# Kernel tuning notes

Measured on AMD Instinct MI355X. Metric: run time of the kernel, lower is better.

Reference implementation:

```python
import jax, jax.numpy as jnp
import numpy as np

N = 2048          # recurrent units (args_dict['n'])
B = 128           # batch
T = 1024          # timesteps
INHIB_PROP = 0.2  # args_dict['inhib_proportion']
SAT_LO, SAT_HI = 0.0, 1.0e8  # saturations -> effectively ReLU


def setup_inputs() -> dict:
    key = jax.random.key(0)
    ks = jax.random.split(key, 8)
    std = 1.0 / np.sqrt(N)
    x0 = jax.random.normal(ks[0], (B, T), jnp.float32)
    x1 = jax.random.normal(ks[1], (B, T), jnp.float32)
    enc0 = jax.random.normal(ks[2], (N,), jnp.float32) * std
    enc1 = jax.random.normal(ks[3], (N,), jnp.float32) * std
    dec0 = jax.random.normal(ks[4], (N,), jnp.float32) * std
    dec1 = jax.random.normal(ks[5], (N,), jnp.float32) * std
    # Dale constraint: W must be elementwise non-negative (asserted in integrate).
    # Scale 1/N keeps the effective spectral radius < 1 for a stable recurrence.
    W = jax.random.uniform(ks[6], (N, N), jnp.float32) * (1.0 / N)
    n_inhib = int(N * INHIB_PROP)
    signs = jnp.concatenate([jnp.ones(N - n_inhib, jnp.float32),
                             -jnp.ones(n_inhib, jnp.float32)])
    mask = jnp.ones((N,), jnp.float32)
    state0 = jnp.zeros((N,), jnp.float32)
    return {"x0": x0, "x1": x1, "enc0": enc0, "enc1": enc1,
            "dec0": dec0, "dec1": dec1, "W": W, "signs": signs,
            "mask": mask, "state0": state0}


def reference(x0, x1, enc0, enc1, dec0, dec1, W, signs, mask, state0):
    # Effective recurrent matrix: W @ diag(signs); state update uses its transpose.
    Weff_T = (W * signs[None, :]).T  # [N, N]

    def step(state, xt):  # state: [B, N]
        i0, i1 = xt  # each [B]
        ext = enc0[None, :] * i0[:, None] + enc1[None, :] * i1[:, None]  # [B, N]
        new_state = mask * jnp.clip((state + mask * ext) @ Weff_T, SAT_LO, SAT_HI)
        o0 = (dec0 * new_state).sum(-1)  # [B]
        o1 = (dec1 * new_state).sum(-1)  # [B]
        return new_state, (o0, o1)

    init = jnp.broadcast_to(state0, (x0.shape[0], state0.shape[0]))  # [B, N]
    _, (o0, o1) = jax.lax.scan(step, init, (x0.T, x1.T))  # outputs [T, B]
    return o0.T, o1.T  # each [B, T]
```

## Files before the change

### kernel.cpp

```cpp
#include <hip/hip_runtime.h>
#include <hip/hip_bf16.h>
#include <stdint.h>


#define NN 2048
#define BB 128
#define TT 1024

typedef __attribute__((ext_vector_type(8)))  __bf16          bf16x8;
typedef __attribute__((ext_vector_type(8)))  unsigned short  ushort8;
typedef __attribute__((ext_vector_type(16))) float           f32x16;

#define IF_OFF   0u
#define IF_FRAGS 32768
#define CTR_OFF  (1u << 20)
#define CTR_BYTES (1024u * 4u * 16u * 4u)

__device__ __forceinline__ unsigned short f2bf(float f) {
    __hip_bfloat16 h = __float2bfloat16(f);
    return *reinterpret_cast<unsigned short*>(&h);
}

__global__ void init_pack(const float* __restrict__ x0, const float* __restrict__ x1,
                          const float* __restrict__ enc0, const float* __restrict__ enc1,
                          const float* __restrict__ mask, const float* __restrict__ state0,
                          unsigned short* __restrict__ If)
{
    int idx  = blockIdx.x * 256 + threadIdx.x;
    int e    = idx & 7;
    int lane = (idx >> 3) & 63;
    int kt   = (idx >> 9) & 127;
    int p    = idx >> 16;
    int b    = p * 32 + (lane & 31);
    int j    = kt * 16 + ((lane >> 5) << 3) + e;
    float v  = state0[j] + mask[j] * (enc0[j] * x0[(size_t)b * TT]
                                    + enc1[j] * x1[(size_t)b * TT]);
    If[idx] = f2bf(v);
}

#define LDS_TOTAL 153856

__global__ void __launch_bounds__(512, 2)
dale_persistent(const float* __restrict__ x0, const float* __restrict__ x1,
                const float* __restrict__ enc0, const float* __restrict__ enc1,
                const float* __restrict__ dec0, const float* __restrict__ dec1,
                const float* __restrict__ W, const float* __restrict__ signs,
                const float* __restrict__ mask,
                unsigned short* __restrict__ If,
                unsigned int* __restrict__ ctr,
                float* __restrict__ out)
{
    extern __shared__ char lds[];
    float* red   = reinterpret_cast<float*>(lds + 131072);
    float* nsbuf = reinterpret_cast<float*>(lds + 131072 + 17408);
    float* ldsC  = reinterpret_cast<float*>(lds + 131072 + 17408 + 4352);
    float* xbuf  = reinterpret_cast<float*>(lds + 131072 + 17408 + 4352 + 768);

    const int tid  = threadIdx.x;
    const int wave = tid >> 6;
    const int lane = tid & 63;
    const int wg   = blockIdx.x;
    const int p  = (wg & 7) >> 1;
    const int q  = ((wg & 1) << 5) | (wg >> 3);
    const int b0 = p * 32;
    const int i0 = q * 32;

    for (int o = tid; o < 8192; o += 512) {
        int il = o >> 8;
        int k8 = o & 255;
        const float* wr = W + (size_t)(i0 + il) * NN + k8 * 8;
        const float* sg = signs + k8 * 8;
        ushort8 pk;
        #pragma unroll
        for (int e = 0; e < 8; ++e) pk[e] = f2bf(wr[e] * sg[e]);
        int slot = k8 ^ il;
        *reinterpret_cast<ushort8*>(lds + il * 4096 + slot * 16) = pk;
    }
    if (tid < 32) {
        ldsC[tid]       = mask[i0 + tid];
        ldsC[32 + tid]  = dec0[i0 + tid];
        ldsC[64 + tid]  = dec1[i0 + tid];
        ldsC[96 + tid]  = enc0[i0 + tid];
        ldsC[128 + tid] = enc1[i0 + tid];
    }
    __syncthreads();

    const bf16x8* Ifrag = reinterpret_cast<const bf16x8*>(If);
    const int il = lane & 31;
    const int hi = lane >> 5;
    char* wrow = lds + il * 4096;

    for (int t = 0; t < TT; ++t) {
        const int par = t & 1;

        bf16x8 A[16];
        const bf16x8* ap = Ifrag + (size_t)par * IF_FRAGS
                         + (p * 128 + wave * 16) * 64 + lane;
        #pragma unroll
        for (int it = 0; it < 16; ++it) {
            const bf16x8* aptr = ap + it * 64;
            asm volatile("global_load_dwordx4 %0, %1, off sc0 sc1"
                         : "=v"(A[it]) : "v"(aptr) : "memory");
        }

        if (tid < 64) {
            int bb = tid & 31;
            const float* xs = (tid < 32) ? x0 : x1;
            float v = (t + 1 < TT) ? xs[(size_t)(b0 + bb) * TT + (t + 1)] : 0.f;
            xbuf[(tid >> 5) * 32 + bb] = v;
        }

        asm volatile("s_waitcnt vmcnt(0)" ::: "memory");
        __builtin_amdgcn_sched_barrier(0);

        f32x16 acc;
        #pragma unroll
        for (int r = 0; r < 16; ++r) acc[r] = 0.f;
        #pragma unroll
        for (int it = 0; it < 16; ++it) {
            int kt   = wave * 16 + it;
            int slot = (kt * 2 + hi) ^ il;
            bf16x8 b = *reinterpret_cast<const bf16x8*>(wrow + slot * 16);
            acc = __builtin_amdgcn_mfma_f32_32x32x16_bf16(A[it], b, acc, 0, 0, 0);
        }

        if (wave >= 4) {
            float* d = red + (wave - 4) * 1088 + lane * 17;
            #pragma unroll
            for (int r = 0; r < 16; ++r) d[r] = acc[r];
        }
        __syncthreads();
        if (wave < 4) {
            const float* s = red + wave * 1088 + lane * 17;
            #pragma unroll
            for (int r = 0; r < 16; ++r) acc[r] += s[r];
        }
        __syncthreads();
        if (wave == 2 || wave == 3) {
            float* d = red + (wave - 2) * 1088 + lane * 17;
            #pragma unroll
            for (int r = 0; r < 16; ++r) d[r] = acc[r];
        }
        __syncthreads();
        if (wave < 2) {
            const float* s = red + wave * 1088 + lane * 17;
            #pragma unroll
            for (int r = 0; r < 16; ++r) acc[r] += s[r];
        }
        __syncthreads();
        if (wave == 1) {
            float* d = red + lane * 17;
            #pragma unroll
            for (int r = 0; r < 16; ++r) d[r] = acc[r];
        }
        __syncthreads();
        if (wave == 0) {
            const float* s = red + lane * 17;
            float mk = ldsC[il];
            #pragma unroll
            for (int r = 0; r < 16; ++r) {
                float raw  = acc[r] + s[r];
                int   brow = (r & 3) + 8 * (r >> 2) + 4 * hi;
                float ns   = fminf(fmaxf(raw, 0.f), 1e8f) * mk;
                nsbuf[brow * 34 + il] = ns;
            }
        }
        __syncthreads();

        int eb = tid >> 4;
        int ei = (tid & 15) * 2;
        float ns0 = nsbuf[eb * 34 + ei];
        float ns1 = nsbuf[eb * 34 + ei + 1];
        float o0p = ldsC[32 + ei] * ns0 + ldsC[32 + ei + 1] * ns1;
        float o1p = ldsC[64 + ei] * ns0 + ldsC[64 + ei + 1] * ns1;
        #pragma unroll
        for (int m = 8; m >= 1; m >>= 1) {
            o0p += __shfl_xor(o0p, m);
            o1p += __shfl_xor(o1p, m);
        }
        if (t + 1 < TT) {
            float xb0 = xbuf[eb], xb1 = xbuf[32 + eb];
            float v0 = ns0 + ldsC[ei]     * (ldsC[96 + ei]     * xb0 + ldsC[128 + ei]     * xb1);
            float v1 = ns1 + ldsC[ei + 1] * (ldsC[96 + ei + 1] * xb0 + ldsC[128 + ei + 1] * xb1);
            int j0 = i0 + ei;
            int kt = j0 >> 4, hb = (j0 >> 3) & 1, e = j0 & 7;
            int fl = eb | (hb << 5);
            unsigned int packed = (unsigned int)f2bf(v0)
                                | ((unsigned int)f2bf(v1) << 16);
            unsigned int* dst = reinterpret_cast<unsigned int*>(If)
                + ((((unsigned)(1 - par)) * IF_FRAGS + (p * 128 + kt) * 64 + fl) * 8 + e) / 2;
            asm volatile("global_store_dword %0, %1, off sc0 sc1"
                         :: "v"(dst), "v"(packed) : "memory");
        }

        asm volatile("s_waitcnt vmcnt(0)" ::: "memory");
        __syncthreads();
        if (tid == 0) {
            unsigned int* cp = ctr + ((unsigned)t * 4u + (unsigned)p) * 16u;
            __hip_atomic_fetch_add(cp, 1u, __ATOMIC_RELAXED, __HIP_MEMORY_SCOPE_AGENT);
            int guard = 0;
            while (__hip_atomic_load(cp, __ATOMIC_RELAXED, __HIP_MEMORY_SCOPE_AGENT) < 64u
                   && ++guard < (1 << 18)) {
                __builtin_amdgcn_s_sleep(1);
            }
        }
        __syncthreads();

        if ((tid & 15) == 0) {
            atomicAdd(out + (size_t)(b0 + eb) * TT + t, o0p);
            atomicAdd(out + (size_t)BB * TT + (size_t)(b0 + eb) * TT + t, o1p);
        }
    }
}

extern "C" void kernel_launch(void* const* d_in, const int* in_sizes, int n_in,
                              void* d_out, int out_size, void* d_ws, size_t ws_size,
                              hipStream_t stream)
{
    (void)in_sizes; (void)n_in; (void)ws_size;
    const float* x0    = (const float*)d_in[0];
    const float* x1    = (const float*)d_in[1];
    const float* enc0  = (const float*)d_in[2];
    const float* enc1  = (const float*)d_in[3];
    const float* dec0  = (const float*)d_in[4];
    const float* dec1  = (const float*)d_in[5];
    const float* W     = (const float*)d_in[6];
    const float* signs = (const float*)d_in[7];
    const float* mask  = (const float*)d_in[8];
    const float* st0   = (const float*)d_in[9];

    unsigned short* If  = (unsigned short*)((char*)d_ws + IF_OFF);
    unsigned int*   ctr = (unsigned int*)((char*)d_ws + CTR_OFF);
    float*          out = (float*)d_out;

    hipMemsetAsync(d_out, 0, sizeof(float) * (size_t)out_size, stream);
    hipMemsetAsync(ctr, 0, CTR_BYTES, stream);

    init_pack<<<1024, 256, 0, stream>>>(x0, x1, enc0, enc1, mask, st0, If);

    hipFuncSetAttribute(reinterpret_cast<const void*>(&dale_persistent),
                        hipFuncAttributeMaxDynamicSharedMemorySize, LDS_TOTAL);
    dale_persistent<<<256, 512, LDS_TOTAL, stream>>>(
        x0, x1, enc0, enc1, dec0, dec1, W, signs, mask, If, ctr, out);
}
```

Measured before the change: 7.144 ms.

## Replace global barrier with per-wave dataflow counters and shorten reduction

Replaces the per-step all-workgroup barrier, where thread 0 spins after every step, with per-slice arrival counters. Each wave waits only for the 16 producer workgroups whose state chunk it reads, and two waves publish their results directly with short stores before bumping the counter. It also splits the A-fragment wait into two halves so MFMAs can start sooner, and cuts the LDS reduction from five barriers to two. The risks are correctness of memory ordering with relaxed atomics and the cost of many 2-byte scattered stores.

```diff
diff --git a/kernel.cpp b/kernel.cpp
--- a/kernel.cpp
+++ b/kernel.cpp
@@ -14,7 +14,7 @@
 #define IF_OFF   0u
 #define IF_FRAGS 32768
 #define CTR_OFF  (1u << 20)
-#define CTR_BYTES (1024u * 4u * 16u * 4u)
+#define CTR_BYTES 2048u
 
 __device__ __forceinline__ unsigned short f2bf(float f) {
     __hip_bfloat16 h = __float2bfloat16(f);
@@ -66,15 +66,15 @@
     const int i0 = q * 32;
 
     for (int o = tid; o < 8192; o += 512) {
-        int il = o >> 8;
-        int k8 = o & 255;
-        const float* wr = W + (size_t)(i0 + il) * NN + k8 * 8;
+        int il8 = o >> 8;
+        int k8  = o & 255;
+        const float* wr = W + (size_t)(i0 + il8) * NN + k8 * 8;
         const float* sg = signs + k8 * 8;
         ushort8 pk;
         #pragma unroll
         for (int e = 0; e < 8; ++e) pk[e] = f2bf(wr[e] * sg[e]);
-        int slot = k8 ^ il;
-        *reinterpret_cast<ushort8*>(lds + il * 4096 + slot * 16) = pk;
+        int slot = k8 ^ il8;
+        *reinterpret_cast<ushort8*>(lds + il8 * 4096 + slot * 16) = pk;
     }
     if (tid < 32) {
         ldsC[tid]       = mask[i0 + tid];
@@ -85,17 +85,58 @@
     }
     __syncthreads();
 
-    const bf16x8* Ifrag = reinterpret_cast<const bf16x8*>(If);
     const int il = lane & 31;
     const int hi = lane >> 5;
     char* wrow = lds + il * 4096;
 
+    const bf16x8* ApBase = reinterpret_cast<const bf16x8*>(If)
+                         + (p * 128 + wave * 16) * 64 + lane;
+    unsigned int* waitCtr = ctr + ((p * 8 + wave) << 4);
+    unsigned int* arrCtr  = ctr + ((p * 8 + (q >> 3)) << 4);
+
+    const float mk  = ldsC[il];
+    const float e0c = ldsC[96 + il];
+    const float e1c = ldsC[128 + il];
+    const int jl   = i0 + il;
+    const int kt_l = jl >> 4;
+    const int hb_l = (jl >> 3) & 1;
+    const int e_l  = jl & 7;
+    unsigned short* sb0 = If + ((size_t)(p * 128 + kt_l) * 64) * 8 + e_l + hb_l * 256;
+    unsigned short* sb1 = sb0 + (size_t)IF_FRAGS * 8;
+
+    const int eb = tid >> 4;
+    const int ei = (tid & 15) * 2;
+    const float d00 = ldsC[32 + ei], d01 = ldsC[32 + ei + 1];
+    const float d10 = ldsC[64 + ei], d11 = ldsC[64 + ei + 1];
+    float* out0 = out + (size_t)(b0 + eb) * TT;
+    float* out1 = out + (size_t)BB * TT + (size_t)(b0 + eb) * TT;
+
     for (int t = 0; t < TT; ++t) {
         const int par = t & 1;
 
+        if (t > 0) {
+            const unsigned tgt = 16u * (unsigned)t;
+            int guard = 0;
+            for (;;) {
+                unsigned vv = 0;
+                if (lane == 0)
+                    vv = __hip_atomic_load(waitCtr, __ATOMIC_RELAXED,
+                                           __HIP_MEMORY_SCOPE_AGENT);
+                unsigned v = (unsigned)__shfl((int)vv, 0, 64);
+                if (v >= tgt || ++guard >= (1 << 17)) break;
+                __builtin_amdgcn_s_sleep(1);
+            }
+        }
+
+        if (wave == 0) {
+            int bb = lane & 31;
+            const float* xs = (lane < 32) ? x0 : x1;
+            float v = (t + 1 < TT) ? xs[(size_t)(b0 + bb) * TT + (t + 1)] : 0.f;
+            xbuf[hi * 32 + bb] = v;
+        }
+
         bf16x8 A[16];
-        const bf16x8* ap = Ifrag + (size_t)par * IF_FRAGS
-                         + (p * 128 + wave * 16) * 64 + lane;
+        const bf16x8* ap = ApBase + (size_t)par * IF_FRAGS;
         #pragma unroll
         for (int it = 0; it < 16; ++it) {
             const bf16x8* aptr = ap + it * 64;
@@ -103,26 +144,28 @@
                          : "=v"(A[it]) : "v"(aptr) : "memory");
         }
 
-        if (tid < 64) {
-            int bb = tid & 31;
-            const float* xs = (tid < 32) ? x0 : x1;
-            float v = (t + 1 < TT) ? xs[(size_t)(b0 + bb) * TT + (t + 1)] : 0.f;
-            xbuf[(tid >> 5) * 32 + bb] = v;
-        }
-
-        asm volatile("s_waitcnt vmcnt(0)" ::: "memory");
+        f32x16 acc;
+        #pragma unroll
+        for (int r = 0; r < 16; ++r) acc[r] = 0.f;
+
+        asm volatile("s_waitcnt vmcnt(8)" ::: "memory");
         __builtin_amdgcn_sched_barrier(0);
-
-        f32x16 acc;
-        #pragma unroll
-        for (int r = 0; r < 16; ++r) acc[r] = 0.f;
-        #pragma unroll
-        for (int it = 0; it < 16; ++it) {
+        #pragma unroll
+        for (int it = 0; it < 8; ++it) {
             int kt   = wave * 16 + it;
             int slot = (kt * 2 + hi) ^ il;
             bf16x8 b = *reinterpret_cast<const bf16x8*>(wrow + slot * 16);
             acc = __builtin_amdgcn_mfma_f32_32x32x16_bf16(A[it], b, acc, 0, 0, 0);
         }
+        asm volatile("s_waitcnt vmcnt(0)" ::: "memory");
+        __builtin_amdgcn_sched_barrier(0);
+        #pragma unroll
+        for (int it = 8; it < 16; ++it) {
+            int kt   = wave * 16 + it;
+            int slot = (kt * 2 + hi) ^ il;
+            bf16x8 b = *reinterpret_cast<const bf16x8*>(wrow + slot * 16);
+            acc = __builtin_amdgcn_mfma_f32_32x32x16_bf16(A[it], b, acc, 0, 0, 0);
+        }
 
         if (wave >= 4) {
             float* d = red + (wave - 4) * 1088 + lane * 17;
@@ -134,81 +177,71 @@
             const float* s = red + wave * 1088 + lane * 17;
             #pragma unroll
             for (int r = 0; r < 16; ++r) acc[r] += s[r];
-        }
-        __syncthreads();
-        if (wave == 2 || wave == 3) {
-            float* d = red + (wave - 2) * 1088 + lane * 17;
-            #pragma unroll
-            for (int r = 0; r < 16; ++r) d[r] = acc[r];
-        }
-        __syncthreads();
+            if (wave >= 2) {
+                float* d = red + wave * 1088 + lane * 17;
+                #pragma unroll
+                for (int r = 0; r < 16; ++r) d[r] = acc[r];
+            }
+        }
+        __syncthreads();
+        if (wave == 0) {
+            const float* s = red + 2 * 1088 + lane * 17;
+            #pragma unroll
+            for (int r = 0; r < 16; ++r) acc[r] += s[r];
+            float* d = red + lane * 17;
+            #pragma unroll
+            for (int rr = 0; rr < 8; ++rr) d[rr] = acc[8 + rr];
+        } else if (wave == 1) {
+            const float* s = red + 3 * 1088 + lane * 17;
+            #pragma unroll
+            for (int r = 0; r < 16; ++r) acc[r] += s[r];
+            float* d = red + 1088 + lane * 17;
+            #pragma unroll
+            for (int rr = 0; rr < 8; ++rr) d[rr] = acc[rr];
+        }
+        __syncthreads();
+
         if (wave < 2) {
-            const float* s = red + wave * 1088 + lane * 17;
-            #pragma unroll
-            for (int r = 0; r < 16; ++r) acc[r] += s[r];
-        }
-        __syncthreads();
-        if (wave == 1) {
-            float* d = red + lane * 17;
-            #pragma unroll
-            for (int r = 0; r < 16; ++r) d[r] = acc[r];
-        }
-        __syncthreads();
-        if (wave == 0) {
-            const float* s = red + lane * 17;
-            float mk = ldsC[il];
-            #pragma unroll
-            for (int r = 0; r < 16; ++r) {
-                float raw  = acc[r] + s[r];
+            const float* s = red + (1 ^ wave) * 1088 + lane * 17;
+            unsigned short* sb = (par == 0) ? sb1 : sb0;
+            #pragma unroll
+            for (int rr = 0; rr < 8; ++rr) {
+                int   r    = (wave << 3) + rr;
+                float raw  = acc[r] + s[rr];
                 int   brow = (r & 3) + 8 * (r >> 2) + 4 * hi;
                 float ns   = fminf(fmaxf(raw, 0.f), 1e8f) * mk;
                 nsbuf[brow * 34 + il] = ns;
-            }
-        }
-        __syncthreads();
-
-        int eb = tid >> 4;
-        int ei = (tid & 15) * 2;
-        float ns0 = nsbuf[eb * 34 + ei];
-        float ns1 = nsbuf[eb * 34 + ei + 1];
-        float o0p = ldsC[32 + ei] * ns0 + ldsC[32 + ei + 1] * ns1;
-        float o1p = ldsC[64 + ei] * ns0 + ldsC[64 + ei + 1] * ns1;
-        #pragma unroll
-        for (int m = 8; m >= 1; m >>= 1) {
-            o0p += __shfl_xor(o0p, m);
-            o1p += __shfl_xor(o1p, m);
-        }
-        if (t + 1 < TT) {
-            float xb0 = xbuf[eb], xb1 = xbuf[32 + eb];
-            float v0 = ns0 + ldsC[ei]     * (ldsC[96 + ei]     * xb0 + ldsC[128 + ei]     * xb1);
-            float v1 = ns1 + ldsC[ei + 1] * (ldsC[96 + ei + 1] * xb0 + ldsC[128 + ei + 1] * xb1);
-            int j0 = i0 + ei;
-            int kt = j0 >> 4, hb = (j0 >> 3) & 1, e = j0 & 7;
-            int fl = eb | (hb << 5);
-            unsigned int packed = (unsigned int)f2bf(v0)
-                                | ((unsigned int)f2bf(v1) << 16);
-            unsigned int* dst = reinterpret_cast<unsigned int*>(If)
-                + ((((unsigned)(1 - par)) * IF_FRAGS + (p * 128 + kt) * 64 + fl) * 8 + e) / 2;
-            asm volatile("global_store_dword %0, %1, off sc0 sc1"
-                         :: "v"(dst), "v"(packed) : "memory");
-        }
-
-        asm volatile("s_waitcnt vmcnt(0)" ::: "memory");
-        __syncthreads();
-        if (tid == 0) {
-            unsigned int* cp = ctr + ((unsigned)t * 4u + (unsigned)p) * 16u;
-            __hip_atomic_fetch_add(cp, 1u, __ATOMIC_RELAXED, __HIP_MEMORY_SCOPE_AGENT);
-            int guard = 0;
-            while (__hip_atomic_load(cp, __ATOMIC_RELAXED, __HIP_MEMORY_SCOPE_AGENT) < 64u
-                   && ++guard < (1 << 18)) {
-                __builtin_amdgcn_s_sleep(1);
-            }
-        }
-        __syncthreads();
-
-        if ((tid & 15) == 0) {
-            atomicAdd(out + (size_t)(b0 + eb) * TT + t, o0p);
-            atomicAdd(out + (size_t)BB * TT + (size_t)(b0 + eb) * TT + t, o1p);
+                if (t + 1 < TT) {
+                    float v = ns + mk * (e0c * xbuf[brow] + e1c * xbuf[32 + brow]);
+                    unsigned int pv = (unsigned int)f2bf(v);
+                    const unsigned short* dst = sb + brow * 8;
+                    asm volatile("global_store_short %0, %1, off sc0 sc1"
+                                 :: "v"(dst), "v"(pv) : "memory");
+                }
+            }
+            if (t + 1 < TT) {
+                asm volatile("s_waitcnt vmcnt(0)" ::: "memory");
+                if (lane == 0)
+                    __hip_atomic_fetch_add(arrCtr, 1u, __ATOMIC_RELAXED,
+                                           __HIP_MEMORY_SCOPE_AGENT);
+            }
+        }
+        __syncthreads();
+
+        {
+            float ns0 = nsbuf[eb * 34 + ei];
+            float ns1 = nsbuf[eb * 34 + ei + 1];
+            float o0p = d00 * ns0 + d01 * ns1;
+            float o1p = d10 * ns0 + d11 * ns1;
+            #pragma unroll
+            for (int m = 8; m >= 1; m >>= 1) {
+                o0p += __shfl_xor(o0p, m);
+                o1p += __shfl_xor(o1p, m);
+            }
+            if ((tid & 15) == 0) {
+                atomicAdd(out0 + t, o0p);
+                atomicAdd(out1 + t, o1p);
+            }
         }
     }
 }
```

Measured after the change: 6.979 ms. 1.02x faster.
